# Kernel optimization log

Hardware: AMD Instinct MI355X
Metric: run time of the kernel (lower is better)

The kernel has to match this reference:

```python
import jax, jax.numpy as jnp
import numpy as np

B, S, D, K = 8, 2048, 1024, 256
LN_EPS = 1e-5


def _freq_positions(input_dim, num_freq, spec_len):
    # torch.linspace(0, input_dim//2, num_freq).long(), clamped to rfft length
    pos = np.linspace(0.0, input_dim // 2, num_freq).astype(np.int64)
    return np.clip(pos, 0, spec_len - 1)


def setup_inputs() -> dict:
    key = jax.random.key(0)
    k1, k2, k3 = jax.random.split(key, 3)
    x = jax.random.normal(k1, (B, S, D), dtype=jnp.float32)
    # magnitude init: init_magnitude=0.1 (small jitter keeps gradients non-degenerate)
    magnitude = 0.1 + 0.01 * jax.random.normal(k2, (K, D), dtype=jnp.float32)
    phase = 0.1 * jax.random.normal(k3, (K, D), dtype=jnp.float32)
    interference_w = 0.01 * jax.random.normal(jax.random.fold_in(key, 7), (K, K), dtype=jnp.float32)
    ln_gamma = jnp.ones((D,), dtype=jnp.float32)
    ln_beta = jnp.zeros((D,), dtype=jnp.float32)
    return {"x": x, "magnitude": magnitude, "phase": phase,
            "interference_w": interference_w, "ln_gamma": ln_gamma, "ln_beta": ln_beta}


def reference(x, magnitude, phase, interference_w, ln_gamma, ln_beta):
    b, s, d = x.shape
    residual = x
    padded_len = 1 << int(np.ceil(np.log2(s)))  # static
    if padded_len > s:
        x = jnp.pad(x, ((0, 0), (0, padded_len - s), (0, 0)))
    # FFT along sequence axis: (B, padded_len//2+1, D) complex
    x_fft = jnp.fft.rfft(x, axis=1)
    freq_pos = _freq_positions(d, magnitude.shape[0], x_fft.shape[1])  # (K,) static ints

    # gather selected frequencies: (B, K, D)
    x_selected = x_fft[:, freq_pos, :]
    # complex weights from magnitude/phase
    cw = (magnitude * jnp.cos(phase) + 1j * magnitude * jnp.sin(phase)).astype(jnp.complex64)
    x_weighted = x_selected * cw[None, :, :]
    # interference on real part: bkd,kj->bjd
    interference = jnp.einsum('bkd,kj->bjd', jnp.real(x_weighted), interference_w)
    x_processed = x_weighted + 0.1 * interference.astype(jnp.complex64)

    # scatter back (positions are unique for these dims)
    x_fft_processed = x_fft.at[:, freq_pos, :].set(x_processed)
    x_rec = jnp.fft.irfft(x_fft_processed, n=padded_len, axis=1)[:, :s, :]

    # residual + LayerNorm over last dim (dropout is identity in eval)
    y = x_rec + residual
    mu = jnp.mean(y, axis=-1, keepdims=True)
    var = jnp.mean(jnp.square(y - mu), axis=-1, keepdims=True)
    y = (y - mu) * jax.lax.rsqrt(var + LN_EPS)
    return y * ln_gamma + ln_beta
```

## Files before the change

kernel.cpp:

```cpp
#include <hip/hip_runtime.h>
#include <math.h>

#define NS 2048
#define ND 1024
#define NK 256
#define NB 8

typedef __attribute__((ext_vector_type(8))) short short8;
typedef __attribute__((ext_vector_type(4))) float f32x4;
typedef __attribute__((ext_vector_type(4))) unsigned short u16x4;
typedef __attribute__((ext_vector_type(8))) unsigned short u16x8;

__device__ __forceinline__ unsigned short f2bf(float x) {
  unsigned int u = __float_as_uint(x);
  u = (u + 0x7fffu + ((u >> 16) & 1u)) >> 16;
  return (unsigned short)u;
}
__device__ __forceinline__ float bf2f(unsigned short h) {
  return __uint_as_float(((unsigned int)h) << 16);
}

__device__ __forceinline__ int fpos(int k) {
  return (k == 255) ? 512 : (int)((float)k * (512.0f / 255.0f));
}

__device__ __forceinline__ void gll16(const unsigned short* g, unsigned short* l) {
  __builtin_amdgcn_global_load_lds(
      (__attribute__((address_space(1))) void*)(void*)const_cast<unsigned short*>(g),
      (__attribute__((address_space(3))) void*)l, 16, 0, 0);
}

__global__ __launch_bounds__(256) void k_tab(unsigned short* __restrict__ CF,
                                             unsigned short* __restrict__ CS) {
  int gid = blockIdx.x * 256 + threadIdx.x;
  if (gid < 512 * 2048) {
    int m = gid >> 11, s = gid & 2047;
    int ph = (fpos(m & 255) * s) & 2047;
    float th = (float)ph * 0.0030679615757712823f;
    float v = (m < 256) ? cosf(th) : -sinf(th);
    CF[gid] = f2bf(v);
  } else {
    int g = gid - 512 * 2048;
    int s = g >> 9, kk = g & 511;
    int ph = (fpos(kk & 255) * s) & 2047;
    float th = (float)ph * 0.0030679615757712823f;
    float v = (kk < 256) ? cosf(th) : -sinf(th);
    CS[g] = f2bf(v);
  }
}

__global__ __launch_bounds__(256) void k_cwT(const float* __restrict__ mag,
                                             const float* __restrict__ ph,
                                             float* __restrict__ mcT,
                                             float* __restrict__ msT) {
  int bid = blockIdx.x;
  int kt = bid >> 4, dt = bid & 15;
  int t = threadIdx.x;
  __shared__ float lc[64][68], ls[64][68];
  int kl = t >> 4, d4 = (t & 15) * 4;
#pragma unroll
  for (int i = 0; i < 4; i++) {
    int k = i * 16 + kl;
    size_t off = (size_t)(kt * 64 + k) * ND + dt * 64 + d4;
    float4 mg = *(const float4*)&mag[off];
    float4 pp = *(const float4*)&ph[off];
    float m[4] = {mg.x, mg.y, mg.z, mg.w}, p[4] = {pp.x, pp.y, pp.z, pp.w};
#pragma unroll
    for (int q = 0; q < 4; q++) {
      float sp, cp;
      sincosf(p[q], &sp, &cp);
      lc[k][d4 + q] = m[q] * cp;
      ls[k][d4 + q] = m[q] * sp;
    }
  }
  __syncthreads();
  int dl = t >> 2, kc = (t & 3) * 16;
#pragma unroll
  for (int i = 0; i < 16; i += 4) {
    float4 vc = {lc[kc + i][dl], lc[kc + i + 1][dl], lc[kc + i + 2][dl], lc[kc + i + 3][dl]};
    float4 vs = {ls[kc + i][dl], ls[kc + i + 1][dl], ls[kc + i + 2][dl], ls[kc + i + 3][dl]};
    size_t o = (size_t)(dt * 64 + dl) * 256 + kt * 64 + kc + i;
    *(float4*)&mcT[o] = vc;
    *(float4*)&msT[o] = vs;
  }
}

__global__ __launch_bounds__(256) void k_wt(const float* __restrict__ W,
                                            unsigned short* __restrict__ WT) {
  int bid = blockIdx.x;
  int kt = bid >> 2, jt = bid & 3;
  int t = threadIdx.x;
  __shared__ float lw[64][68];
  int kl = t >> 4, j4 = (t & 15) * 4;
#pragma unroll
  for (int i = 0; i < 4; i++) {
    int k = i * 16 + kl;
    float4 wv = *(const float4*)&W[(size_t)(kt * 64 + k) * 256 + jt * 64 + j4];
    lw[k][j4 + 0] = wv.x; lw[k][j4 + 1] = wv.y;
    lw[k][j4 + 2] = wv.z; lw[k][j4 + 3] = wv.w;
  }
  __syncthreads();
  int jl = t >> 2, kc = (t & 3) * 16;
#pragma unroll
  for (int i = 0; i < 16; i += 4) {
    u16x4 v = {f2bf(lw[kc + i][jl]), f2bf(lw[kc + i + 1][jl]),
               f2bf(lw[kc + i + 2][jl]), f2bf(lw[kc + i + 3][jl])};
    *(u16x4*)&WT[(size_t)(jt * 64 + jl) * 256 + kt * 64 + kc + i] = v;
  }
}

__global__ __launch_bounds__(256) void k_conv(const float* __restrict__ x,
                                              unsigned short* __restrict__ xt) {
  int bid = blockIdx.x;
  int b = bid >> 9, rem = bid & 511;
  int s0 = (rem >> 4) * 64, d0 = (rem & 15) * 64;
  int t = threadIdx.x;
  __shared__ __attribute__((aligned(16))) unsigned short lt[64 * 72];
#pragma unroll
  for (int c = 0; c < 4; c++) {
    int e = c * 256 + t;
    int row = e >> 4, col = (e & 15) * 4;
    float4 v = *(const float4*)&x[((size_t)b * NS + s0 + row) * ND + d0 + col];
    lt[(col + 0) * 72 + row] = f2bf(v.x);
    lt[(col + 1) * 72 + row] = f2bf(v.y);
    lt[(col + 2) * 72 + row] = f2bf(v.z);
    lt[(col + 3) * 72 + row] = f2bf(v.w);
  }
  __syncthreads();
  int dl = t >> 2, sc = (t & 3) * 16;
  u16x8 a = *(u16x8*)&lt[dl * 72 + sc];
  u16x8 bb = *(u16x8*)&lt[dl * 72 + sc + 8];
  size_t o = ((size_t)b * ND + d0 + dl) * NS + s0 + sc;
  *(u16x8*)&xt[o] = a;
  *(u16x8*)&xt[o + 8] = bb;
}

template <int BM, int BN, int OUTT>
__global__ __launch_bounds__(256) void gemm97(const unsigned short* __restrict__ A,
                                              const unsigned short* __restrict__ B,
                                              unsigned short* __restrict__ C,
                                              int M, int N, int K,
                                              size_t sA, size_t sB) {
  constexpr int MI = BM / 32, NI = BN / 32;
  const int mt = M / BM, nt = N / BN;
  int bid = blockIdx.x;
  int b = bid / (mt * nt), r = bid % (mt * nt);
  int m0 = (r / nt) * BM, n0 = (r % nt) * BN;
  int t = threadIdx.x, lane = t & 63, w = t >> 6;
  int wr = (t >> 7) & 1, wc = (t >> 6) & 1;
  __shared__ __attribute__((aligned(16))) unsigned short As[BM * 64];
  __shared__ __attribute__((aligned(16))) unsigned short Bs[BN * 64];
  const unsigned short* Ag = A + b * sA + (size_t)m0 * K;
  const unsigned short* Bg = B + b * sB + (size_t)n0 * K;
  int arow = lane >> 3, ak = (lane & 7) * 8;

  f32x4 acc[MI][NI];
#pragma unroll
  for (int i = 0; i < MI; i++)
#pragma unroll
    for (int j = 0; j < NI; j++) acc[i][j] = {0.f, 0.f, 0.f, 0.f};

  for (int kt = 0; kt < K / 64; kt++) {
    int kofs = kt * 64;
#pragma unroll
    for (int i = 0; i < BM / 32; i++) {
      int r0 = w * (BM / 4) + i * 8;
      gll16(Ag + (size_t)(r0 + arow) * K + kofs + ak, &As[r0 * 64]);
    }
#pragma unroll
    for (int i = 0; i < BN / 32; i++) {
      int r0 = w * (BN / 4) + i * 8;
      gll16(Bg + (size_t)(r0 + arow) * K + kofs + ak, &Bs[r0 * 64]);
    }
    __syncthreads();
#pragma unroll
    for (int ks = 0; ks < 2; ks++) {
      short8 af[MI], bfv[NI];
#pragma unroll
      for (int mi = 0; mi < MI; mi++) {
        int row = wr * (BM / 2) + mi * 16 + (lane & 15);
        af[mi] = *(const short8*)&As[row * 64 + (ks * 4 + (lane >> 4)) * 8];
      }
#pragma unroll
      for (int ni = 0; ni < NI; ni++) {
        int row = wc * (BN / 2) + ni * 16 + (lane & 15);
        bfv[ni] = *(const short8*)&Bs[row * 64 + (ks * 4 + (lane >> 4)) * 8];
      }
#pragma unroll
      for (int mi = 0; mi < MI; mi++)
#pragma unroll
        for (int ni = 0; ni < NI; ni++)
          acc[mi][ni] = __builtin_amdgcn_mfma_f32_16x16x32_bf16(
              af[mi], bfv[ni], acc[mi][ni], 0, 0, 0);
    }
    __syncthreads();
  }

#pragma unroll
  for (int mi = 0; mi < MI; mi++) {
#pragma unroll
    for (int ni = 0; ni < NI; ni++) {
      int row0 = m0 + wr * (BM / 2) + mi * 16 + ((lane >> 4) * 4);
      int col = n0 + wc * (BN / 2) + ni * 16 + (lane & 15);
      if (OUTT == 1) {
        u16x4 v = {f2bf(acc[mi][ni][0]), f2bf(acc[mi][ni][1]),
                   f2bf(acc[mi][ni][2]), f2bf(acc[mi][ni][3])};
        *(u16x4*)&C[((size_t)b * N + col) * M + row0] = v;
      } else {
#pragma unroll
        for (int q = 0; q < 4; q++)
          C[((size_t)b * M + row0 + q) * N + col] = f2bf(acc[mi][ni][q]);
      }
    }
  }
}

__global__ __launch_bounds__(256) void k1bT(const unsigned short* __restrict__ XqT,
                                            const float* __restrict__ mcT,
                                            const float* __restrict__ msT,
                                            unsigned short* __restrict__ RXwT) {
  int gid = blockIdx.x * 256 + threadIdx.x;
  int rw = gid >> 5;
  int k0 = (gid & 31) * 8;
  int d = rw & 1023;
  u16x8 re = *(const u16x8*)&XqT[(size_t)rw * 512 + k0];
  u16x8 im = *(const u16x8*)&XqT[(size_t)rw * 512 + 256 + k0];
  float4 c0 = *(const float4*)&mcT[d * 256 + k0];
  float4 c1 = *(const float4*)&mcT[d * 256 + k0 + 4];
  float4 s0 = *(const float4*)&msT[d * 256 + k0];
  float4 s1 = *(const float4*)&msT[d * 256 + k0 + 4];
  float cc[8] = {c0.x, c0.y, c0.z, c0.w, c1.x, c1.y, c1.z, c1.w};
  float ss[8] = {s0.x, s0.y, s0.z, s0.w, s1.x, s1.y, s1.z, s1.w};
  u16x8 o;
#pragma unroll
  for (int q = 0; q < 8; q++)
    o[q] = f2bf(cc[q] * bf2f(re[q]) - ss[q] * bf2f(im[q]));
  *(u16x8*)&RXwT[(size_t)rw * 256 + k0] = o;
}

__global__ __launch_bounds__(256) void k2b(const unsigned short* __restrict__ IT,
                                           const unsigned short* __restrict__ XqT,
                                           const float* __restrict__ mcT,
                                           const float* __restrict__ msT,
                                           unsigned short* __restrict__ DltT) {
  int gid = blockIdx.x * 256 + threadIdx.x;
  int rw = gid >> 5;
  int j0 = (gid & 31) * 8;
  int d = rw & 1023;
  u16x8 iv = *(const u16x8*)&IT[(size_t)rw * 256 + j0];
  u16x8 re = *(const u16x8*)&XqT[(size_t)rw * 512 + j0];
  u16x8 im = *(const u16x8*)&XqT[(size_t)rw * 512 + 256 + j0];
  float4 c0 = *(const float4*)&mcT[d * 256 + j0];
  float4 c1 = *(const float4*)&mcT[d * 256 + j0 + 4];
  float4 s0 = *(const float4*)&msT[d * 256 + j0];
  float4 s1 = *(const float4*)&msT[d * 256 + j0 + 4];
  float cc[8] = {c0.x, c0.y, c0.z, c0.w, c1.x, c1.y, c1.z, c1.w};
  float ss[8] = {s0.x, s0.y, s0.z, s0.w, s1.x, s1.y, s1.z, s1.w};
  u16x8 orv, oiv;
#pragma unroll
  for (int q = 0; q < 8; q++) {
    int j = j0 + q;
    float alpha = ((j == 0) ? 1.0f : 2.0f) * (1.0f / 2048.0f);
    float xr = bf2f(re[q]), xi = bf2f(im[q]), ii = bf2f(iv[q]);
    float m1 = cc[q] - 1.0f;
    orv[q] = f2bf(alpha * (m1 * xr - ss[q] * xi + 0.1f * ii));
    oiv[q] = f2bf(alpha * (ss[q] * xr + m1 * xi));
  }
  *(u16x8*)&DltT[(size_t)rw * 512 + j0] = orv;
  *(u16x8*)&DltT[(size_t)rw * 512 + 256 + j0] = oiv;
}

__global__ __launch_bounds__(256) void k4_ln(const float* __restrict__ x,
                                             const unsigned short* __restrict__ corr,
                                             const float* __restrict__ g,
                                             const float* __restrict__ be,
                                             float* __restrict__ out) {
  int row = blockIdx.x;
  int t = threadIdx.x;
  size_t base = (size_t)row * ND + t * 4;
  u16x4 cv = *(const u16x4*)&corr[base];
  float4 xv = *(const float4*)&x[base];
  float v[4] = {fmaf(2.f, xv.x, bf2f(cv[0])), fmaf(2.f, xv.y, bf2f(cv[1])),
                fmaf(2.f, xv.z, bf2f(cv[2])), fmaf(2.f, xv.w, bf2f(cv[3]))};
  float s = v[0] + v[1] + v[2] + v[3];
  float q = v[0] * v[0] + v[1] * v[1] + v[2] * v[2] + v[3] * v[3];
#pragma unroll
  for (int o = 32; o >= 1; o >>= 1) {
    s += __shfl_xor(s, o, 64);
    q += __shfl_xor(q, o, 64);
  }
  __shared__ float ss[4], qs[4];
  if ((t & 63) == 0) { ss[t >> 6] = s; qs[t >> 6] = q; }
  __syncthreads();
  s = ss[0] + ss[1] + ss[2] + ss[3];
  q = qs[0] + qs[1] + qs[2] + qs[3];
  float mu = s * (1.0f / (float)ND);
  float var = q * (1.0f / (float)ND) - mu * mu;
  float rstd = rsqrtf(var + 1e-5f);
  float4 gv = *(const float4*)&g[t * 4];
  float4 bv = *(const float4*)&be[t * 4];
  float4 ov;
  ov.x = (v[0] - mu) * rstd * gv.x + bv.x;
  ov.y = (v[1] - mu) * rstd * gv.y + bv.y;
  ov.z = (v[2] - mu) * rstd * gv.z + bv.z;
  ov.w = (v[3] - mu) * rstd * gv.w + bv.w;
  *(float4*)&out[base] = ov;
}

extern "C" void kernel_launch(void* const* d_in, const int* in_sizes, int n_in,
                              void* d_out, int out_size, void* d_ws, size_t ws_size,
                              hipStream_t stream) {
  const float* x   = (const float*)d_in[0];
  const float* mag = (const float*)d_in[1];
  const float* ph  = (const float*)d_in[2];
  const float* W   = (const float*)d_in[3];
  const float* g   = (const float*)d_in[4];
  const float* be  = (const float*)d_in[5];
  float* out = (float*)d_out;
  char* w = (char*)d_ws;

  unsigned short* CF   = (unsigned short*)(w);
  unsigned short* CS   = (unsigned short*)(w + (2ull << 20));
  float*          mcT  = (float*)(w + (4ull << 20));
  float*          msT  = (float*)(w + (5ull << 20));
  unsigned short* WT   = (unsigned short*)(w + (6ull << 20));
  unsigned short* XqT  = (unsigned short*)(w + (7ull << 20));
  unsigned short* RXwT = (unsigned short*)(w + (15ull << 20));
  unsigned short* IT   = (unsigned short*)(w + (19ull << 20));
  unsigned short* DltT = (unsigned short*)(w + (23ull << 20));
  unsigned short* corr = (unsigned short*)(w + (31ull << 20));
  unsigned short* xt   = (unsigned short*)(w + (63ull << 20));

  k_tab<<<8192, 256, 0, stream>>>(CF, CS);
  k_cwT<<<64, 256, 0, stream>>>(mag, ph, mcT, msT);
  k_wt<<<16, 256, 0, stream>>>(W, WT);
  k_conv<<<4096, 256, 0, stream>>>(x, xt);
  gemm97<128, 64, 1><<<512, 256, 0, stream>>>(CF, xt, XqT, 512, 1024, 2048,
                                              0, (size_t)1024 * 2048);
  k1bT<<<1024, 256, 0, stream>>>(XqT, mcT, msT, RXwT);
  gemm97<128, 64, 0><<<256, 256, 0, stream>>>(RXwT, WT, IT, 1024, 256, 256,
                                              (size_t)1024 * 256, 0);
  k2b<<<1024, 256, 0, stream>>>(IT, XqT, mcT, msT, DltT);
  gemm97<128, 128, 0><<<1024, 256, 0, stream>>>(CS, DltT, corr, 2048, 1024, 512,
                                                0, (size_t)1024 * 512);
  k4_ln<<<16384, 256, 0, stream>>>(x, corr, g, be, out);
}
```

Measured before the change: 239.4 us.

## Double-buffer GEMM loads and fuse complex weighting into GEMM epilogues

The bf16 MFMA GEMM now double-buffers its LDS tiles with async global-to-LDS loads and explicit vmcnt waits, so the next K-tile loads while the current one is computed. The two elementwise kernels (complex weighting and delta computation) are folded into the GEMM epilogues, and the DFT tables are interleaved re/im so each lane holds a real/imag pair. The twiddle tables are now built from a 2048-entry double-precision cosine table instead of calling cosf/sinf per element. This removes two launches and their round trips of intermediate tensors through memory, at the cost of scattered 4-byte epilogue accesses and more LDS per block.

```diff
diff --git a/kernel.cpp b/kernel.cpp
--- a/kernel.cpp
+++ b/kernel.cpp
@@ -10,6 +10,7 @@
 typedef __attribute__((ext_vector_type(4))) float f32x4;
 typedef __attribute__((ext_vector_type(4))) unsigned short u16x4;
 typedef __attribute__((ext_vector_type(8))) unsigned short u16x8;
+typedef unsigned int u32;
 
 __device__ __forceinline__ unsigned short f2bf(float x) {
   unsigned int u = __float_as_uint(x);
@@ -30,27 +31,34 @@
       (__attribute__((address_space(3))) void*)l, 16, 0, 0);
 }
 
-__global__ __launch_bounds__(256) void k_tab(unsigned short* __restrict__ CF,
-                                             unsigned short* __restrict__ CS) {
+__global__ __launch_bounds__(256) void k_master(float* __restrict__ master) {
+  int t = blockIdx.x * 256 + threadIdx.x;
+  double th = (double)t * (6.283185307179586476925286766559 / 2048.0);
+  master[t] = (float)cos(th);
+}
+
+__global__ __launch_bounds__(256) void k_tabs(const float* __restrict__ master,
+                                              unsigned short* __restrict__ CFi,
+                                              unsigned short* __restrict__ CSi) {
   int gid = blockIdx.x * 256 + threadIdx.x;
   if (gid < 512 * 2048) {
-    int m = gid >> 11, s = gid & 2047;
-    int ph = (fpos(m & 255) * s) & 2047;
-    float th = (float)ph * 0.0030679615757712823f;
-    float v = (m < 256) ? cosf(th) : -sinf(th);
-    CF[gid] = f2bf(v);
+    int r = gid >> 11, s = gid & 2047;
+    int p = (fpos(r >> 1) * s) & 2047;
+    float v = (r & 1) ? -master[(p + 1536) & 2047] : master[p];
+    CFi[gid] = f2bf(v);
   } else {
     int g = gid - 512 * 2048;
-    int s = g >> 9, kk = g & 511;
-    int ph = (fpos(kk & 255) * s) & 2047;
-    float th = (float)ph * 0.0030679615757712823f;
-    float v = (kk < 256) ? cosf(th) : -sinf(th);
-    CS[g] = f2bf(v);
-  }
-}
-
-__global__ __launch_bounds__(256) void k_cwT(const float* __restrict__ mag,
+    int s = g >> 9, c = g & 511;
+    int p = (fpos(c >> 1) * s) & 2047;
+    float v = (c & 1) ? -master[(p + 1536) & 2047] : master[p];
+    CSi[g] = f2bf(v);
+  }
+}
+
+__global__ __launch_bounds__(256) void k_cw2(const float* __restrict__ mag,
                                              const float* __restrict__ ph,
+                                             float* __restrict__ mc,
+                                             float* __restrict__ ms,
                                              float* __restrict__ mcT,
                                              float* __restrict__ msT) {
   int bid = blockIdx.x;
@@ -65,13 +73,21 @@
     float4 mg = *(const float4*)&mag[off];
     float4 pp = *(const float4*)&ph[off];
     float m[4] = {mg.x, mg.y, mg.z, mg.w}, p[4] = {pp.x, pp.y, pp.z, pp.w};
+    float4 vc, vs;
+    float oc[4], os[4];
 #pragma unroll
     for (int q = 0; q < 4; q++) {
       float sp, cp;
       sincosf(p[q], &sp, &cp);
-      lc[k][d4 + q] = m[q] * cp;
-      ls[k][d4 + q] = m[q] * sp;
+      oc[q] = m[q] * cp;
+      os[q] = m[q] * sp;
+      lc[k][d4 + q] = oc[q];
+      ls[k][d4 + q] = os[q];
     }
+    vc = make_float4(oc[0], oc[1], oc[2], oc[3]);
+    vs = make_float4(os[0], os[1], os[2], os[3]);
+    *(float4*)&mc[off] = vc;
+    *(float4*)&ms[off] = vs;
   }
   __syncthreads();
   int dl = t >> 2, kc = (t & 3) * 16;
@@ -135,21 +151,25 @@
   *(u16x8*)&xt[o + 8] = bb;
 }
 
-template <int BM, int BN, int OUTT>
-__global__ __launch_bounds__(256) void gemm97(const unsigned short* __restrict__ A,
-                                              const unsigned short* __restrict__ B,
-                                              unsigned short* __restrict__ C,
-                                              int M, int N, int K,
-                                              size_t sA, size_t sB) {
+template <int BM, int BN, int EPI>
+__global__ __launch_bounds__(256) void gemm_db(const unsigned short* __restrict__ A,
+                                               const unsigned short* __restrict__ B,
+                                               unsigned short* __restrict__ C0,
+                                               unsigned short* __restrict__ C1,
+                                               const float* __restrict__ P0,
+                                               const float* __restrict__ P1,
+                                               int M, int N, int K,
+                                               size_t sA, size_t sB) {
   constexpr int MI = BM / 32, NI = BN / 32;
+  constexpr int NSTG = (BM + BN) / 32;
   const int mt = M / BM, nt = N / BN;
   int bid = blockIdx.x;
   int b = bid / (mt * nt), r = bid % (mt * nt);
   int m0 = (r / nt) * BM, n0 = (r % nt) * BN;
   int t = threadIdx.x, lane = t & 63, w = t >> 6;
   int wr = (t >> 7) & 1, wc = (t >> 6) & 1;
-  __shared__ __attribute__((aligned(16))) unsigned short As[BM * 64];
-  __shared__ __attribute__((aligned(16))) unsigned short Bs[BN * 64];
+  __shared__ __attribute__((aligned(16))) unsigned short As[2][BM * 64];
+  __shared__ __attribute__((aligned(16))) unsigned short Bs[2][BN * 64];
   const unsigned short* Ag = A + b * sA + (size_t)m0 * K;
   const unsigned short* Bg = B + b * sB + (size_t)n0 * K;
   int arow = lane >> 3, ak = (lane & 7) * 8;
@@ -160,31 +180,43 @@
 #pragma unroll
     for (int j = 0; j < NI; j++) acc[i][j] = {0.f, 0.f, 0.f, 0.f};
 
-  for (int kt = 0; kt < K / 64; kt++) {
-    int kofs = kt * 64;
-#pragma unroll
-    for (int i = 0; i < BM / 32; i++) {
-      int r0 = w * (BM / 4) + i * 8;
-      gll16(Ag + (size_t)(r0 + arow) * K + kofs + ak, &As[r0 * 64]);
-    }
-#pragma unroll
-    for (int i = 0; i < BN / 32; i++) {
-      int r0 = w * (BN / 4) + i * 8;
-      gll16(Bg + (size_t)(r0 + arow) * K + kofs + ak, &Bs[r0 * 64]);
-    }
-    __syncthreads();
+  const int nkt = K / 64;
+
+#define STAGE(buf, kt_)                                                      \
+  do {                                                                       \
+    int kofs = (kt_) * 64;                                                   \
+    _Pragma("unroll") for (int i = 0; i < BM / 32; i++) {                    \
+      int r0 = w * (BM / 4) + i * 8;                                         \
+      gll16(Ag + (size_t)(r0 + arow) * K + kofs + ak, &As[buf][r0 * 64]);    \
+    }                                                                        \
+    _Pragma("unroll") for (int i = 0; i < BN / 32; i++) {                    \
+      int r0 = w * (BN / 4) + i * 8;                                         \
+      gll16(Bg + (size_t)(r0 + arow) * K + kofs + ak, &Bs[buf][r0 * 64]);    \
+    }                                                                        \
+  } while (0)
+
+  STAGE(0, 0);
+  if (nkt > 1) STAGE(1, 1);
+
+  for (int kt = 0; kt < nkt; kt++) {
+    int cur = kt & 1;
+    if (kt + 1 < nkt)
+      asm volatile("s_waitcnt vmcnt(%0)" ::"n"(NSTG) : "memory");
+    else
+      asm volatile("s_waitcnt vmcnt(0)" ::: "memory");
+    __builtin_amdgcn_s_barrier();
 #pragma unroll
     for (int ks = 0; ks < 2; ks++) {
       short8 af[MI], bfv[NI];
 #pragma unroll
       for (int mi = 0; mi < MI; mi++) {
         int row = wr * (BM / 2) + mi * 16 + (lane & 15);
-        af[mi] = *(const short8*)&As[row * 64 + (ks * 4 + (lane >> 4)) * 8];
+        af[mi] = *(const short8*)&As[cur][row * 64 + (ks * 4 + (lane >> 4)) * 8];
       }
 #pragma unroll
       for (int ni = 0; ni < NI; ni++) {
         int row = wc * (BN / 2) + ni * 16 + (lane & 15);
-        bfv[ni] = *(const short8*)&Bs[row * 64 + (ks * 4 + (lane >> 4)) * 8];
+        bfv[ni] = *(const short8*)&Bs[cur][row * 64 + (ks * 4 + (lane >> 4)) * 8];
       }
 #pragma unroll
       for (int mi = 0; mi < MI; mi++)
@@ -193,8 +225,10 @@
           acc[mi][ni] = __builtin_amdgcn_mfma_f32_16x16x32_bf16(
               af[mi], bfv[ni], acc[mi][ni], 0, 0, 0);
     }
-    __syncthreads();
-  }
+    __builtin_amdgcn_s_barrier();
+    if (kt + 2 < nkt) STAGE(cur, kt + 2);
+  }
+#undef STAGE
 
 #pragma unroll
   for (int mi = 0; mi < MI; mi++) {
@@ -202,72 +236,38 @@
     for (int ni = 0; ni < NI; ni++) {
       int row0 = m0 + wr * (BM / 2) + mi * 16 + ((lane >> 4) * 4);
       int col = n0 + wc * (BN / 2) + ni * 16 + (lane & 15);
-      if (OUTT == 1) {
-        u16x4 v = {f2bf(acc[mi][ni][0]), f2bf(acc[mi][ni][1]),
-                   f2bf(acc[mi][ni][2]), f2bf(acc[mi][ni][3])};
-        *(u16x4*)&C[((size_t)b * N + col) * M + row0] = v;
+      f32x4 a = acc[mi][ni];
+      if (EPI == 0) {
+#pragma unroll
+        for (int q = 0; q < 4; q++)
+          C0[((size_t)b * M + row0 + q) * N + col] = f2bf(a[q]);
+      } else if (EPI == 1) {
+        u16x4 xv = {f2bf(a[0]), f2bf(a[1]), f2bf(a[2]), f2bf(a[3])};
+        *(u16x4*)&C0[((size_t)b * N + col) * M + row0] = xv;
+        int j0 = row0 >> 1, j1 = j0 + 1;
+        float rw0 = P0[(size_t)j0 * ND + col] * a[0] - P1[(size_t)j0 * ND + col] * a[1];
+        float rw1 = P0[(size_t)j1 * ND + col] * a[2] - P1[(size_t)j1 * ND + col] * a[3];
+        u32 pk = (u32)f2bf(rw0) | ((u32)f2bf(rw1) << 16);
+        *(u32*)&C1[((size_t)b * N + col) * (M / 2) + j0] = pk;
       } else {
-#pragma unroll
-        for (int q = 0; q < 4; q++)
-          C[((size_t)b * M + row0 + q) * N + col] = f2bf(acc[mi][ni][q]);
+        float alpha = ((col == 0) ? 1.0f : 2.0f) * (1.0f / 2048.0f);
+#pragma unroll
+        for (int q = 0; q < 4; q++) {
+          int dd = row0 + q;
+          u32 reim = *(const u32*)&C1[((size_t)b * M + dd) * 512 + 2 * col];
+          float xr = bf2f((unsigned short)(reim & 0xffffu));
+          float xi = bf2f((unsigned short)(reim >> 16));
+          float mcv = P0[(size_t)dd * 256 + col];
+          float msv = P1[(size_t)dd * 256 + col];
+          float m1 = mcv - 1.0f;
+          float dre = alpha * (m1 * xr - msv * xi + 0.1f * a[q]);
+          float dim = alpha * (msv * xr + m1 * xi);
+          u32 pk = (u32)f2bf(dre) | ((u32)f2bf(dim) << 16);
+          *(u32*)&C0[((size_t)b * M + dd) * 512 + 2 * col] = pk;
+        }
       }
     }
   }
-}
-
-__global__ __launch_bounds__(256) void k1bT(const unsigned short* __restrict__ XqT,
-                                            const float* __restrict__ mcT,
-                                            const float* __restrict__ msT,
-                                            unsigned short* __restrict__ RXwT) {
-  int gid = blockIdx.x * 256 + threadIdx.x;
-  int rw = gid >> 5;
-  int k0 = (gid & 31) * 8;
-  int d = rw & 1023;
-  u16x8 re = *(const u16x8*)&XqT[(size_t)rw * 512 + k0];
-  u16x8 im = *(const u16x8*)&XqT[(size_t)rw * 512 + 256 + k0];
-  float4 c0 = *(const float4*)&mcT[d * 256 + k0];
-  float4 c1 = *(const float4*)&mcT[d * 256 + k0 + 4];
-  float4 s0 = *(const float4*)&msT[d * 256 + k0];
-  float4 s1 = *(const float4*)&msT[d * 256 + k0 + 4];
-  float cc[8] = {c0.x, c0.y, c0.z, c0.w, c1.x, c1.y, c1.z, c1.w};
-  float ss[8] = {s0.x, s0.y, s0.z, s0.w, s1.x, s1.y, s1.z, s1.w};
-  u16x8 o;
-#pragma unroll
-  for (int q = 0; q < 8; q++)
-    o[q] = f2bf(cc[q] * bf2f(re[q]) - ss[q] * bf2f(im[q]));
-  *(u16x8*)&RXwT[(size_t)rw * 256 + k0] = o;
-}
-
-__global__ __launch_bounds__(256) void k2b(const unsigned short* __restrict__ IT,
-                                           const unsigned short* __restrict__ XqT,
-                                           const float* __restrict__ mcT,
-                                           const float* __restrict__ msT,
-                                           unsigned short* __restrict__ DltT) {
-  int gid = blockIdx.x * 256 + threadIdx.x;
-  int rw = gid >> 5;
-  int j0 = (gid & 31) * 8;
-  int d = rw & 1023;
-  u16x8 iv = *(const u16x8*)&IT[(size_t)rw * 256 + j0];
-  u16x8 re = *(const u16x8*)&XqT[(size_t)rw * 512 + j0];
-  u16x8 im = *(const u16x8*)&XqT[(size_t)rw * 512 + 256 + j0];
-  float4 c0 = *(const float4*)&mcT[d * 256 + j0];
-  float4 c1 = *(const float4*)&mcT[d * 256 + j0 + 4];
-  float4 s0 = *(const float4*)&msT[d * 256 + j0];
-  float4 s1 = *(const float4*)&msT[d * 256 + j0 + 4];
-  float cc[8] = {c0.x, c0.y, c0.z, c0.w, c1.x, c1.y, c1.z, c1.w};
-  float ss[8] = {s0.x, s0.y, s0.z, s0.w, s1.x, s1.y, s1.z, s1.w};
-  u16x8 orv, oiv;
-#pragma unroll
-  for (int q = 0; q < 8; q++) {
-    int j = j0 + q;
-    float alpha = ((j == 0) ? 1.0f : 2.0f) * (1.0f / 2048.0f);
-    float xr = bf2f(re[q]), xi = bf2f(im[q]), ii = bf2f(iv[q]);
-    float m1 = cc[q] - 1.0f;
-    orv[q] = f2bf(alpha * (m1 * xr - ss[q] * xi + 0.1f * ii));
-    oiv[q] = f2bf(alpha * (ss[q] * xr + m1 * xi));
-  }
-  *(u16x8*)&DltT[(size_t)rw * 512 + j0] = orv;
-  *(u16x8*)&DltT[(size_t)rw * 512 + 256 + j0] = oiv;
 }
 
 __global__ __launch_bounds__(256) void k4_ln(const float* __restrict__ x,
@@ -319,29 +319,34 @@
   float* out = (float*)d_out;
   char* w = (char*)d_ws;
 
-  unsigned short* CF   = (unsigned short*)(w);
-  unsigned short* CS   = (unsigned short*)(w + (2ull << 20));
-  float*          mcT  = (float*)(w + (4ull << 20));
-  float*          msT  = (float*)(w + (5ull << 20));
-  unsigned short* WT   = (unsigned short*)(w + (6ull << 20));
-  unsigned short* XqT  = (unsigned short*)(w + (7ull << 20));
-  unsigned short* RXwT = (unsigned short*)(w + (15ull << 20));
-  unsigned short* IT   = (unsigned short*)(w + (19ull << 20));
-  unsigned short* DltT = (unsigned short*)(w + (23ull << 20));
-  unsigned short* corr = (unsigned short*)(w + (31ull << 20));
-  unsigned short* xt   = (unsigned short*)(w + (63ull << 20));
-
-  k_tab<<<8192, 256, 0, stream>>>(CF, CS);
-  k_cwT<<<64, 256, 0, stream>>>(mag, ph, mcT, msT);
+  float*          master = (float*)(w);
+  unsigned short* CFi    = (unsigned short*)(w + (1ull << 20));
+  unsigned short* CSi    = (unsigned short*)(w + (3ull << 20));
+  float*          mc     = (float*)(w + (5ull << 20));
+  float*          ms     = (float*)(w + (6ull << 20));
+  float*          mcT    = (float*)(w + (7ull << 20));
+  float*          msT    = (float*)(w + (8ull << 20));
+  unsigned short* WT     = (unsigned short*)(w + (9ull << 20));
+  unsigned short* XqT    = (unsigned short*)(w + (10ull << 20));
+  unsigned short* RXwT   = (unsigned short*)(w + (18ull << 20));
+  unsigned short* DltT   = (unsigned short*)(w + (22ull << 20));
+  unsigned short* corr   = (unsigned short*)(w + (30ull << 20));
+  unsigned short* xt     = (unsigned short*)(w + (62ull << 20));
+
+  k_master<<<8, 256, 0, stream>>>(master);
+  k_tabs<<<8192, 256, 0, stream>>>(master, CFi, CSi);
+  k_cw2<<<64, 256, 0, stream>>>(mag, ph, mc, ms, mcT, msT);
   k_wt<<<16, 256, 0, stream>>>(W, WT);
   k_conv<<<4096, 256, 0, stream>>>(x, xt);
-  gemm97<128, 64, 1><<<512, 256, 0, stream>>>(CF, xt, XqT, 512, 1024, 2048,
-                                              0, (size_t)1024 * 2048);
-  k1bT<<<1024, 256, 0, stream>>>(XqT, mcT, msT, RXwT);
-  gemm97<128, 64, 0><<<256, 256, 0, stream>>>(RXwT, WT, IT, 1024, 256, 256,
-                                              (size_t)1024 * 256, 0);
-  k2b<<<1024, 256, 0, stream>>>(IT, XqT, mcT, msT, DltT);
-  gemm97<128, 128, 0><<<1024, 256, 0, stream>>>(CS, DltT, corr, 2048, 1024, 512,
-                                                0, (size_t)1024 * 512);
+  gemm_db<128, 64, 1><<<512, 256, 0, stream>>>(CFi, xt, XqT, RXwT, mc, ms,
+                                               512, 1024, 2048, 0,
+                                               (size_t)1024 * 2048);
+  gemm_db<128, 64, 2><<<256, 256, 0, stream>>>(RXwT, WT, DltT, XqT, mcT, msT,
+                                               1024, 256, 256,
+                                               (size_t)1024 * 256, 0);
+  gemm_db<128, 128, 0><<<1024, 256, 0, stream>>>(CSi, DltT, corr, nullptr,
+                                                 nullptr, nullptr,
+                                                 2048, 1024, 512, 0,
+                                                 (size_t)1024 * 512);
   k4_ln<<<16384, 256, 0, stream>>>(x, corr, g, be, out);
 }
```

Result: no change. 236.6 us (-1.2%).
